# Optimization experiments

Hardware: AMD Instinct MI355X
Metric: run time of the kernel (lower is better)

Reference implementation:

```python
import jax, jax.numpy as jnp
import numpy as np

T, B, OBS, H, A = 512, 512, 128, 128, 18


def setup_inputs() -> dict:
    key = jax.random.key(0)
    ks = jax.random.split(key, 8)
    return {
        "hidden": jnp.zeros((B, H), jnp.float32),
        "obs": jax.random.normal(ks[0], (T, B, OBS), jnp.float32),
        "dones": jax.random.bernoulli(ks[1], 0.01, (T, B)),
        # embedding Dense (orthogonal-ish scale sqrt(2))
        "W_emb": jax.random.normal(ks[2], (OBS, H), jnp.float32) * (np.sqrt(2.0) / np.sqrt(OBS)).astype(np.float32),
        "b_emb": jnp.zeros((H,), jnp.float32),
        # GRUCell params: input path Wi/bi cover gates [r | z | n]; hidden path Wh (no bias for r,z), bhn for n
        "Wi": jax.random.normal(ks[3], (H, 3 * H), jnp.float32) / np.float32(np.sqrt(H)),
        "bi": jnp.zeros((3 * H,), jnp.float32),
        "Wh": jax.random.normal(ks[4], (H, 3 * H), jnp.float32) / np.float32(np.sqrt(H)),
        "bhn": jnp.zeros((H,), jnp.float32),
        # output Dense to action_dim
        "W_out": jax.random.normal(ks[5], (H, A), jnp.float32) / np.float32(np.sqrt(H)),
        "b_out": jnp.zeros((A,), jnp.float32),
    }


def reference(hidden, obs, dones, W_emb, b_emb, Wi, bi, Wh, bhn, W_out, b_out):
    # Dense embed + relu: [T, B, OBS] -> [T, B, H]
    emb = jax.nn.relu(obs @ W_emb + b_emb)
    # precompute input-path gate pre-activations for all steps: [T, B, 3H]
    gi = emb @ Wi + bi

    def step(h, xs):
        gi_t, reset = xs  # [B, 3H], [B]
        # reset-masked carry: initialize_carry gives zeros
        h = jnp.where(reset[:, None], jnp.zeros_like(h), h)
        gh = h @ Wh  # [B, 3H]
        r = jax.nn.sigmoid(gi_t[:, :H] + gh[:, :H])
        z = jax.nn.sigmoid(gi_t[:, H:2 * H] + gh[:, H:2 * H])
        n = jnp.tanh(gi_t[:, 2 * H:] + r * (gh[:, 2 * H:] + bhn))
        h_new = (1.0 - z) * n + z * h
        return h_new, h_new

    h_final, ys = jax.lax.scan(step, hidden, (gi, dones))  # ys: [T, B, H]
    q_vals = ys @ W_out + b_out  # [T, B, A]
    return (h_final, q_vals)
```

## Files before the change

### kernel.cpp

```cpp
#include <hip/hip_runtime.h>

#define T_DIM 512
#define B_DIM 512
#define OBS_DIM 128
#define H_DIM 128
#define A_DIM 18
#define G3 384
#define LDSS 136
#define K1_ITERS 8

#define SC_R (-1.44269504088896f)
#define SC_N (2.88539008177793f)

typedef _Float16 v8h __attribute__((ext_vector_type(8)));
typedef _Float16 v4h __attribute__((ext_vector_type(4)));
typedef _Float16 v2h __attribute__((ext_vector_type(2)));
typedef float v4f __attribute__((ext_vector_type(4)));
typedef float v2f __attribute__((ext_vector_type(2)));

#define EXP2F(x) __builtin_amdgcn_exp2f(x)
#define RCPF(x)  __builtin_amdgcn_rcpf(x)
#define PKRTZ(a,b) __builtin_bit_cast(v2h, __builtin_amdgcn_cvt_pkrtz((a),(b)))

#define BAR() asm volatile("s_waitcnt lgkmcnt(0)\n\ts_barrier" ::: "memory")

__global__ __launch_bounds__(512, 4) void k1_embed_gi(
    const float* __restrict__ obs,
    const float* __restrict__ W_emb,
    const float* __restrict__ b_emb,
    const float* __restrict__ Wi,
    const float* __restrict__ bi,
    _Float16* __restrict__ gRZ,
    _Float16* __restrict__ gN)
{
    __shared__ __align__(16) _Float16 obs_lds[64 * LDSS];
    __shared__ __align__(16) _Float16 emb_lds[64 * LDSS];
    const int tid  = threadIdx.x;
    const int cg   = tid >> 6;
    const int lane = tid & 63;
    const int n16  = lane & 15;
    const int quad = lane >> 4;

    v8h fe[4];
    v8h fi[3][4];
#pragma unroll
    for (int kt = 0; kt < 4; ++kt)
#pragma unroll
        for (int j = 0; j < 8; ++j) {
            const int k = kt * 32 + quad * 8 + j;
            fe[kt][j] = (_Float16)W_emb[k * H_DIM + cg * 16 + n16];
        }
#pragma unroll
    for (int g = 0; g < 3; ++g) {
        const float sc = (g == 2) ? SC_N : SC_R;
#pragma unroll
        for (int kt = 0; kt < 4; ++kt)
#pragma unroll
            for (int j = 0; j < 8; ++j) {
                const int k = kt * 32 + quad * 8 + j;
                fi[g][kt][j] = (_Float16)(Wi[k * G3 + g * H_DIM + cg * 16 + n16] * sc);
            }
    }
    v4f bemb_c, bir_c, biz_c, bin_c;
#pragma unroll
    for (int r = 0; r < 4; ++r) {
        const int col = cg * 16 + quad * 4 + r;
        bemb_c[r] = b_emb[col];
        bir_c[r]  = bi[col] * SC_R;
        biz_c[r]  = bi[H_DIM + col] * SC_R;
        bin_c[r]  = bi[2 * H_DIM + col] * SC_N;
    }

    const int srow = tid >> 3;
    const int sk   = (tid & 7) * 16;
    const int base = blockIdx.x * K1_ITERS;

    {
        const float* op = obs + (size_t)(base * 64 + srow) * OBS_DIM + sk;
#pragma unroll
        for (int q = 0; q < 4; ++q) {
            const float4 a = *(const float4*)(op + q * 4);
            v4h pa = { (_Float16)a.x, (_Float16)a.y, (_Float16)a.z, (_Float16)a.w };
            *(v4h*)&obs_lds[srow * LDSS + sk + q * 4] = pa;
        }
    }
    __syncthreads();

    for (int i = 0; i < K1_ITERS; ++i) {
        const int row0 = (base + i) * 64;
        const int ni = (i + 1 < K1_ITERS) ? i + 1 : i;
        const float* opn = obs + (size_t)((base + ni) * 64 + srow) * OBS_DIM + sk;
        float4 nv[4];
#pragma unroll
        for (int q = 0; q < 4; ++q) nv[q] = *(const float4*)(opn + q * 4);

#pragma unroll
        for (int rt = 0; rt < 4; ++rt) {
            v8h bo[4];
#pragma unroll
            for (int kt = 0; kt < 4; ++kt)
                bo[kt] = *(const v8h*)&obs_lds[(rt * 16 + n16) * LDSS + kt * 32 + quad * 8];
            v4f ea = bemb_c;
#pragma unroll
            for (int kt = 0; kt < 4; ++kt)
                ea = __builtin_amdgcn_mfma_f32_16x16x32_f16(fe[kt], bo[kt], ea, 0, 0, 0);
            v4h e;
#pragma unroll
            for (int r = 0; r < 4; ++r) e[r] = (_Float16)fmaxf(ea[r], 0.f);
            *(v4h*)&emb_lds[(rt * 16 + n16) * LDSS + cg * 16 + quad * 4] = e;
        }
        BAR();
#pragma unroll
        for (int rt = 0; rt < 4; ++rt) {
            v8h be[4];
#pragma unroll
            for (int kt = 0; kt < 4; ++kt)
                be[kt] = *(const v8h*)&emb_lds[(rt * 16 + n16) * LDSS + kt * 32 + quad * 8];
            v4f ar = bir_c, az = biz_c, an = bin_c;
#pragma unroll
            for (int kt = 0; kt < 4; ++kt) {
                ar = __builtin_amdgcn_mfma_f32_16x16x32_f16(fi[0][kt], be[kt], ar, 0, 0, 0);
                az = __builtin_amdgcn_mfma_f32_16x16x32_f16(fi[1][kt], be[kt], az, 0, 0, 0);
                an = __builtin_amdgcn_mfma_f32_16x16x32_f16(fi[2][kt], be[kt], an, 0, 0, 0);
            }
            const int R = row0 + rt * 16 + n16;
            v8h rz;
#pragma unroll
            for (int r = 0; r < 4; ++r) {
                rz[r]     = (_Float16)ar[r];
                rz[4 + r] = (_Float16)az[r];
            }
            *(v8h*)&gRZ[(size_t)R * 256 + cg * 32 + quad * 8] = rz;
            v4h nn;
#pragma unroll
            for (int r = 0; r < 4; ++r) nn[r] = (_Float16)an[r];
            *(v4h*)&gN[(size_t)R * 128 + cg * 16 + quad * 4] = nn;
        }
#pragma unroll
        for (int q = 0; q < 4; ++q) {
            v4h pa = { (_Float16)nv[q].x, (_Float16)nv[q].y, (_Float16)nv[q].z, (_Float16)nv[q].w };
            *(v4h*)&obs_lds[srow * LDSS + sk + q * 4] = pa;
        }
        BAR();
    }
}

__global__ __launch_bounds__(512) void k2_recurrence(
    const float* __restrict__ hidden,
    const unsigned char* __restrict__ dones_raw,
    const _Float16* __restrict__ gRZ,
    const _Float16* __restrict__ gN,
    const float* __restrict__ Wh,
    const float* __restrict__ bhn,
    const float* __restrict__ W_out,
    const float* __restrict__ b_out,
    float* __restrict__ out)
{
    __shared__ __align__(16) _Float16 h_lds[2][16 * LDSS];
    __shared__ __align__(16) unsigned char d_lds[(T_DIM + 1) * 16];
    __shared__ int byte_mode;
    const int tid  = threadIdx.x;
    const int w    = tid >> 6;
    const int lane = tid & 63;
    const int n16  = lane & 15;
    const int quad = lane >> 4;
    const int c16  = w * 16 + quad * 4;
    const int B0   = blockIdx.x * 16;

    if (tid == 0) byte_mode = 0;
    __syncthreads();
    {
        int hit = 0;
        for (int i = tid; i < 4096; i += 512)
            if ((i & 3) != 0 && dones_raw[i] == 1) hit = 1;
        if (hit) byte_mode = 1;
    }
    __syncthreads();
    const bool bm = (byte_mode != 0);

    {
        if (bm) {
            const int4 v = *(const int4*)(dones_raw + (size_t)tid * B_DIM + B0);
            *(int4*)&d_lds[tid * 16] = v;
        } else {
            const int* di = (const int*)dones_raw;
            const int* pp = di + (size_t)tid * B_DIM + B0;
            int4 wv; unsigned char* wb = (unsigned char*)&wv;
#pragma unroll
            for (int j = 0; j < 16; ++j) wb[j] = (unsigned char)(pp[j] != 0);
            *(int4*)&d_lds[tid * 16] = wv;
        }
        if (tid == 0) { int4 z = {0,0,0,0}; *(int4*)&d_lds[T_DIM * 16] = z; }
    }

    v8h fh[3][4];
#pragma unroll
    for (int g = 0; g < 3; ++g) {
        const float sc = (g == 2) ? SC_N : SC_R;
#pragma unroll
        for (int kt = 0; kt < 4; ++kt)
#pragma unroll
            for (int j = 0; j < 8; ++j) {
                const int k = kt * 32 + quad * 8 + j;
                fh[g][kt][j] = (_Float16)(Wh[k * G3 + g * H_DIM + w * 16 + n16] * sc);
            }
    }
    const v4f bhn_c = { bhn[c16] * SC_N, bhn[c16 + 1] * SC_N,
                        bhn[c16 + 2] * SC_N, bhn[c16 + 3] * SC_N };

    v8h fo[4];
    float bq[4];
    if (w < 2) {
        const int col = w * 16 + n16;
#pragma unroll
        for (int kt = 0; kt < 4; ++kt)
#pragma unroll
            for (int j = 0; j < 8; ++j) {
                const int k = kt * 32 + quad * 8 + j;
                fo[kt][j] = (col < A_DIM) ? (_Float16)W_out[k * A_DIM + col] : (_Float16)0.f;
            }
#pragma unroll
        for (int r = 0; r < 4; ++r) {
            const int c = w * 16 + quad * 4 + r;
            bq[r] = (c < A_DIM) ? b_out[c] : 0.f;
        }
    }
    float* qout = out + (size_t)B_DIM * H_DIM;

    __syncthreads();

    const bool d0 = d_lds[n16] != 0;
    v4f huv;
#pragma unroll
    for (int r = 0; r < 4; ++r) {
        const float hv = hidden[(size_t)(B0 + n16) * H_DIM + c16 + r];
        huv[r] = d0 ? 0.f : hv;
    }
    {
        v2h h01 = PKRTZ(huv[0], huv[1]);
        v2h h23 = PKRTZ(huv[2], huv[3]);
        v4h hw = { h01[0], h01[1], h23[0], h23[1] };
        *(v4h*)&h_lds[0][n16 * LDSS + c16] = hw;
    }

    const int RZB = B_DIM * 256 * 2;
    const int NB  = B_DIM * 128 * 2;
    const int rzo = ((B0 + n16) * 256 + w * 32 + quad * 8) * 2;
    const int no_ = ((B0 + n16) * 128 + c16) * 2;
    const char* gRZc = (const char*)gRZ;
    const char* gNc  = (const char*)gN;

    v8h s8a = *(const v8h*)(gRZc + 0 * (size_t)RZB + rzo);
    v8h s8b = *(const v8h*)(gRZc + 1 * (size_t)RZB + rzo);
    v8h s8c = *(const v8h*)(gRZc + 2 * (size_t)RZB + rzo);
    v8h s8d = *(const v8h*)(gRZc + 3 * (size_t)RZB + rzo);
    v4h s4a = *(const v4h*)(gNc + 0 * (size_t)NB + no_);
    v4h s4b = *(const v4h*)(gNc + 1 * (size_t)NB + no_);
    v4h s4c = *(const v4h*)(gNc + 2 * (size_t)NB + no_);
    v4h s4d = *(const v4h*)(gNc + 3 * (size_t)NB + no_);

    const char* rzb = gRZc + (size_t)4 * RZB;
    const char* nb  = gNc  + (size_t)4 * NB;
    int dpo = 16 + n16;
    bool dprev = false;
    __syncthreads();

    auto STEP = [&](int t, v8h& s8, v4h& s4,
                    const _Float16* __restrict__ hin, _Float16* __restrict__ hout)
        __attribute__((always_inline)) -> void {
        const unsigned char dnx = d_lds[dpo];

        v8h bh[4];
#pragma unroll
        for (int kt = 0; kt < 4; ++kt)
            bh[kt] = *(const v8h*)&hin[n16 * LDSS + kt * 32 + quad * 8];

        if (w < 2) {
            v4f qa = {0.f,0.f,0.f,0.f};
#pragma unroll
            for (int kt = 0; kt < 4; ++kt)
                qa = __builtin_amdgcn_mfma_f32_16x16x32_f16(fo[kt], bh[kt], qa, 0, 0, 0);
            if (t > 0) {
                float* qp = qout + ((size_t)(t - 1) * B_DIM + B0 + n16) * A_DIM;
                const int cbase = w * 16 + quad * 4;
#pragma unroll
                for (int r = 0; r < 4; ++r)
                    if (cbase + r < A_DIM) qp[cbase + r] = qa[r] + bq[r];
            }
        }

        v4f ga0 = {0.f,0.f,0.f,0.f};
#pragma unroll
        for (int kt = 0; kt < 4; ++kt)
            ga0 = __builtin_amdgcn_mfma_f32_16x16x32_f16(fh[0][kt], bh[kt], ga0, 0, 0, 0);
        v4f ga1 = {0.f,0.f,0.f,0.f};
#pragma unroll
        for (int kt = 0; kt < 4; ++kt)
            ga1 = __builtin_amdgcn_mfma_f32_16x16x32_f16(fh[1][kt], bh[kt], ga1, 0, 0, 0);

        if (dprev) { ga0 = (v4f){0.f,0.f,0.f,0.f}; ga1 = (v4f){0.f,0.f,0.f,0.f}; }

        v2f arl = (v2f){ (float)s8[0], (float)s8[1] } + (v2f){ ga0[0], ga0[1] };
        v2f arh = (v2f){ (float)s8[2], (float)s8[3] } + (v2f){ ga0[2], ga0[3] };
        v2f rgl = { RCPF(EXP2F(arl[0]) + 1.f), RCPF(EXP2F(arl[1]) + 1.f) };
        v2f rgh = { RCPF(EXP2F(arh[0]) + 1.f), RCPF(EXP2F(arh[1]) + 1.f) };

        v4f ga2 = bhn_c;
#pragma unroll
        for (int kt = 0; kt < 4; ++kt)
            ga2 = __builtin_amdgcn_mfma_f32_16x16x32_f16(fh[2][kt], bh[kt], ga2, 0, 0, 0);
        if (dprev) ga2 = bhn_c;

        v2f azl = (v2f){ (float)s8[4], (float)s8[5] } + (v2f){ ga1[0], ga1[1] };
        v2f azh = (v2f){ (float)s8[6], (float)s8[7] } + (v2f){ ga1[2], ga1[3] };
        v2f ezl = { EXP2F(azl[0]), EXP2F(azl[1]) };
        v2f ezh = { EXP2F(azh[0]), EXP2F(azh[1]) };

        v2f snl = rgl * (v2f){ ga2[0], ga2[1] } + (v2f){ (float)s4[0], (float)s4[1] };
        v2f snh = rgh * (v2f){ ga2[2], ga2[3] } + (v2f){ (float)s4[2], (float)s4[3] };
        v2f enl = { EXP2F(snl[0]), EXP2F(snl[1]) };
        v2f enh = { EXP2F(snh[0]), EXP2F(snh[1]) };
        v2f enpl = enl + 1.f, enph = enh + 1.f;
        v2f enml = enl - 1.f, enmh = enh - 1.f;
        v2f hul = { huv[0], huv[1] }, huh = { huv[2], huv[3] };
        v2f numl = hul * enpl + enml * ezl;
        v2f numh = huh * enph + enmh * ezh;
        v2f denl = enpl * (ezl + 1.f);
        v2f denh = enph * (ezh + 1.f);
        v2f hnl = numl * (v2f){ RCPF(denl[0]), RCPF(denl[1]) };
        v2f hnh = numh * (v2f){ RCPF(denh[0]), RCPF(denh[1]) };

        v2h y01 = PKRTZ(hnl[0], hnl[1]);
        v2h y23 = PKRTZ(hnh[0], hnh[1]);
        v4h yv = { y01[0], y01[1], y23[0], y23[1] };
        *(v4h*)&hout[n16 * LDSS + c16] = yv;
        const bool dn = dnx != 0;
#pragma unroll
        for (int r = 0; r < 4; ++r) huv[r] = dn ? 0.f : (r < 2 ? hnl[r] : hnh[r - 2]);
        dprev = dn;

        s8 = *(const v8h*)(rzb + rzo);
        s4 = *(const v4h*)(nb + no_);

        if (t < 507) { rzb += RZB; nb += NB; }
        dpo += 16;
        BAR();
    };

    for (int t = 0; t < T_DIM; t += 4) {
        STEP(t,     s8a, s4a, h_lds[0], h_lds[1]);
        STEP(t + 1, s8b, s4b, h_lds[1], h_lds[0]);
        STEP(t + 2, s8c, s4c, h_lds[0], h_lds[1]);
        STEP(t + 3, s8d, s4d, h_lds[1], h_lds[0]);
    }

    if (w < 2) {
        v8h bh[4];
#pragma unroll
        for (int kt = 0; kt < 4; ++kt)
            bh[kt] = *(const v8h*)&h_lds[0][n16 * LDSS + kt * 32 + quad * 8];
        v4f qa = {0.f,0.f,0.f,0.f};
#pragma unroll
        for (int kt = 0; kt < 4; ++kt)
            qa = __builtin_amdgcn_mfma_f32_16x16x32_f16(fo[kt], bh[kt], qa, 0, 0, 0);
        float* qp = qout + ((size_t)(T_DIM - 1) * B_DIM + B0 + n16) * A_DIM;
        const int cbase = w * 16 + quad * 4;
#pragma unroll
        for (int r = 0; r < 4; ++r)
            if (cbase + r < A_DIM) qp[cbase + r] = qa[r] + bq[r];
    }

#pragma unroll
    for (int r = 0; r < 4; ++r)
        out[(size_t)(B0 + n16) * H_DIM + c16 + r] = huv[r];
}

extern "C" void kernel_launch(void* const* d_in, const int* in_sizes, int n_in,
                              void* d_out, int out_size, void* d_ws, size_t ws_size,
                              hipStream_t stream) {
    const float* hidden = (const float*)d_in[0];
    const float* obs    = (const float*)d_in[1];
    const unsigned char* dones = (const unsigned char*)d_in[2];
    const float* W_emb  = (const float*)d_in[3];
    const float* b_emb  = (const float*)d_in[4];
    const float* Wi     = (const float*)d_in[5];
    const float* bi     = (const float*)d_in[6];
    const float* Wh     = (const float*)d_in[7];
    const float* bhn    = (const float*)d_in[8];
    const float* W_out  = (const float*)d_in[9];
    const float* b_out  = (const float*)d_in[10];
    float* out = (float*)d_out;

    _Float16* gRZ = (_Float16*)d_ws;
    _Float16* gN  = gRZ + (size_t)T_DIM * B_DIM * 256;

    hipLaunchKernelGGL(k1_embed_gi, dim3(512), dim3(512), 0, stream,
                       obs, W_emb, b_emb, Wi, bi, gRZ, gN);
    hipLaunchKernelGGL(k2_recurrence, dim3(32), dim3(512), 0, stream,
                       hidden, dones, gRZ, gN, Wh, bhn, W_out, b_out, out);
}
```

Before: 611.3 us.

## Double-buffer embed/gate stages in k1 and halve its grid

Restructures the embedding+gate kernel into a software pipeline: the embedding for tile i+1 is computed into a second LDS buffer while the gate GEMM for tile i runs, so only one barrier per iteration remains. Observations are prefetched two tiles ahead. Each block now handles 16 tiles and the grid drops to 256 blocks, with the occupancy hint removed from launch bounds. This doubles LDS use and may lower occupancy, and k1 is likely a small part of the total time next to the recurrence kernel.

Measured after the change: 591.1 us. 3.3% less time.

```diff
diff --git a/kernel.cpp b/kernel.cpp
--- a/kernel.cpp
+++ b/kernel.cpp
@@ -7,7 +7,7 @@
 #define A_DIM 18
 #define G3 384
 #define LDSS 136
-#define K1_ITERS 8
+#define K1_ITERS 16
 
 #define SC_R (-1.44269504088896f)
 #define SC_N (2.88539008177793f)
@@ -24,7 +24,7 @@
 
 #define BAR() asm volatile("s_waitcnt lgkmcnt(0)\n\ts_barrier" ::: "memory")
 
-__global__ __launch_bounds__(512, 4) void k1_embed_gi(
+__global__ __launch_bounds__(512) void k1_embed_gi(
     const float* __restrict__ obs,
     const float* __restrict__ W_emb,
     const float* __restrict__ b_emb,
@@ -33,8 +33,8 @@
     _Float16* __restrict__ gRZ,
     _Float16* __restrict__ gN)
 {
-    __shared__ __align__(16) _Float16 obs_lds[64 * LDSS];
-    __shared__ __align__(16) _Float16 emb_lds[64 * LDSS];
+    __shared__ __align__(16) _Float16 obs_lds[2][64 * LDSS];
+    __shared__ __align__(16) _Float16 emb_lds[2][64 * LDSS];
     const int tid  = threadIdx.x;
     const int cg   = tid >> 6;
     const int lane = tid & 63;
@@ -81,25 +81,23 @@
         for (int q = 0; q < 4; ++q) {
             const float4 a = *(const float4*)(op + q * 4);
             v4h pa = { (_Float16)a.x, (_Float16)a.y, (_Float16)a.z, (_Float16)a.w };
-            *(v4h*)&obs_lds[srow * LDSS + sk + q * 4] = pa;
+            *(v4h*)&obs_lds[0][srow * LDSS + sk + q * 4] = pa;
         }
     }
     __syncthreads();
 
-    for (int i = 0; i < K1_ITERS; ++i) {
-        const int row0 = (base + i) * 64;
-        const int ni = (i + 1 < K1_ITERS) ? i + 1 : i;
-        const float* opn = obs + (size_t)((base + ni) * 64 + srow) * OBS_DIM + sk;
+    {
+        const float* op1 = obs + (size_t)((base + 1) * 64 + srow) * OBS_DIM + sk;
         float4 nv[4];
 #pragma unroll
-        for (int q = 0; q < 4; ++q) nv[q] = *(const float4*)(opn + q * 4);
+        for (int q = 0; q < 4; ++q) nv[q] = *(const float4*)(op1 + q * 4);
 
 #pragma unroll
         for (int rt = 0; rt < 4; ++rt) {
             v8h bo[4];
 #pragma unroll
             for (int kt = 0; kt < 4; ++kt)
-                bo[kt] = *(const v8h*)&obs_lds[(rt * 16 + n16) * LDSS + kt * 32 + quad * 8];
+                bo[kt] = *(const v8h*)&obs_lds[0][(rt * 16 + n16) * LDSS + kt * 32 + quad * 8];
             v4f ea = bemb_c;
 #pragma unroll
             for (int kt = 0; kt < 4; ++kt)
@@ -107,15 +105,32 @@
             v4h e;
 #pragma unroll
             for (int r = 0; r < 4; ++r) e[r] = (_Float16)fmaxf(ea[r], 0.f);
-            *(v4h*)&emb_lds[(rt * 16 + n16) * LDSS + cg * 16 + quad * 4] = e;
-        }
-        BAR();
+            *(v4h*)&emb_lds[0][(rt * 16 + n16) * LDSS + cg * 16 + quad * 4] = e;
+        }
+#pragma unroll
+        for (int q = 0; q < 4; ++q) {
+            v4h pa = { (_Float16)nv[q].x, (_Float16)nv[q].y, (_Float16)nv[q].z, (_Float16)nv[q].w };
+            *(v4h*)&obs_lds[1][srow * LDSS + sk + q * 4] = pa;
+        }
+    }
+    BAR();
+
+    for (int i = 0; i < K1_ITERS; ++i) {
+        const int cur = i & 1, nxt = cur ^ 1;
+        const int row0 = (base + i) * 64;
+
+        const int pi = (i + 2 < K1_ITERS) ? i + 2 : K1_ITERS - 1;
+        const float* opn = obs + (size_t)((base + pi) * 64 + srow) * OBS_DIM + sk;
+        float4 nv[4];
+#pragma unroll
+        for (int q = 0; q < 4; ++q) nv[q] = *(const float4*)(opn + q * 4);
+
 #pragma unroll
         for (int rt = 0; rt < 4; ++rt) {
             v8h be[4];
 #pragma unroll
             for (int kt = 0; kt < 4; ++kt)
-                be[kt] = *(const v8h*)&emb_lds[(rt * 16 + n16) * LDSS + kt * 32 + quad * 8];
+                be[kt] = *(const v8h*)&emb_lds[cur][(rt * 16 + n16) * LDSS + kt * 32 + quad * 8];
             v4f ar = bir_c, az = biz_c, an = bin_c;
 #pragma unroll
             for (int kt = 0; kt < 4; ++kt) {
@@ -136,10 +151,27 @@
             for (int r = 0; r < 4; ++r) nn[r] = (_Float16)an[r];
             *(v4h*)&gN[(size_t)R * 128 + cg * 16 + quad * 4] = nn;
         }
+
+#pragma unroll
+        for (int rt = 0; rt < 4; ++rt) {
+            v8h bo[4];
+#pragma unroll
+            for (int kt = 0; kt < 4; ++kt)
+                bo[kt] = *(const v8h*)&obs_lds[nxt][(rt * 16 + n16) * LDSS + kt * 32 + quad * 8];
+            v4f ea = bemb_c;
+#pragma unroll
+            for (int kt = 0; kt < 4; ++kt)
+                ea = __builtin_amdgcn_mfma_f32_16x16x32_f16(fe[kt], bo[kt], ea, 0, 0, 0);
+            v4h e;
+#pragma unroll
+            for (int r = 0; r < 4; ++r) e[r] = (_Float16)fmaxf(ea[r], 0.f);
+            *(v4h*)&emb_lds[nxt][(rt * 16 + n16) * LDSS + cg * 16 + quad * 4] = e;
+        }
+
 #pragma unroll
         for (int q = 0; q < 4; ++q) {
             v4h pa = { (_Float16)nv[q].x, (_Float16)nv[q].y, (_Float16)nv[q].z, (_Float16)nv[q].w };
-            *(v4h*)&obs_lds[srow * LDSS + sk + q * 4] = pa;
+            *(v4h*)&obs_lds[cur][srow * LDSS + sk + q * 4] = pa;
         }
         BAR();
     }
@@ -394,7 +426,7 @@
     _Float16* gRZ = (_Float16*)d_ws;
     _Float16* gN  = gRZ + (size_t)T_DIM * B_DIM * 256;
 
-    hipLaunchKernelGGL(k1_embed_gi, dim3(512), dim3(512), 0, stream,
+    hipLaunchKernelGGL(k1_embed_gi, dim3(256), dim3(512), 0, stream,
                        obs, W_emb, b_emb, Wi, bi, gRZ, gN);
     hipLaunchKernelGGL(k2_recurrence, dim3(32), dim3(512), 0, stream,
                        hidden, dones, gRZ, gN, Wh, bhn, W_out, b_out, out);
```
